# Kernel tuning notes

Measured on AMD Instinct MI355X. Metric: run time of the kernel, lower is better.

## Reference

```python
import jax, jax.numpy as jnp
import numpy as np

N_NODES, N_EDGES, N_GRAPHS = 50000, 800000, 128
D_IN, H1, H2, N_CLASSES = 128, 128, 128, 2
NEG_SLOPE = 0.2  # PyG GATConv default


def setup_inputs() -> dict:
    key = jax.random.key(0)
    ks = jax.random.split(key, 12)
    x = jax.random.normal(ks[0], (N_NODES, D_IN), jnp.float32)
    edge_index = jax.random.randint(ks[1], (2, N_EDGES), 0, N_NODES, jnp.int32)
    batch = jnp.sort(jax.random.randint(ks[2], (N_NODES,), 0, N_GRAPHS, jnp.int32))
    s = 0.05
    return {
        "x": x,
        "W1": jax.random.normal(ks[3], (D_IN, H1), jnp.float32) * s,
        "att_src": jax.random.normal(ks[4], (H1,), jnp.float32) * s,
        "att_dst": jax.random.normal(ks[5], (H1,), jnp.float32) * s,
        "b1": jnp.zeros((H1,), jnp.float32),
        "W2": jax.random.normal(ks[6], (H1, H2), jnp.float32) * s,
        "b2": jnp.zeros((H2,), jnp.float32),
        "Wf": jax.random.normal(ks[7], (H2, N_CLASSES), jnp.float32) * s,
        "bf": jnp.zeros((N_CLASSES,), jnp.float32),
        "edge_index": edge_index,
        "batch": batch,
    }


def _add_self_loops(src, dst, n):
    loop = jnp.arange(n, dtype=src.dtype)
    return jnp.concatenate([src, loop]), jnp.concatenate([dst, loop])


def gat_conv(x, W, att_src, att_dst, bias, src, dst, n):
    h = x @ W  # [N, H1]
    a_src = h @ att_src  # [N]
    a_dst = h @ att_dst  # [N]
    e = a_src[src] + a_dst[dst]  # [E']
    e = jnp.where(e > 0, e, NEG_SLOPE * e)  # leaky_relu
    # softmax over incoming edges of each dst node
    m = jax.ops.segment_max(e, dst, num_segments=n)
    ex = jnp.exp(e - m[dst])
    denom = jax.ops.segment_sum(ex, dst, num_segments=n)
    alpha = ex / denom[dst]  # self loops guarantee denom > 0
    out = jax.ops.segment_sum(alpha[:, None] * h[src], dst, num_segments=n)
    return out + bias


def gcn_conv(x, W, bias, src, dst, n):
    h = x @ W  # [N, H2]
    ones = jnp.ones(src.shape[0], h.dtype)
    deg = jax.ops.segment_sum(ones, dst, num_segments=n)
    dinv = jnp.where(deg > 0, jax.lax.rsqrt(deg), 0.0)
    norm = dinv[src] * dinv[dst]  # [E']
    out = jax.ops.segment_sum(norm[:, None] * h[src], dst, num_segments=n)
    return out + bias


def reference(x, W1, att_src, att_dst, b1, W2, b2, Wf, bf, edge_index, batch):
    n = x.shape[0]
    src, dst = _add_self_loops(edge_index[0], edge_index[1], n)
    h = jax.nn.relu(gat_conv(x, W1, att_src, att_dst, b1, src, dst, n))
    h = jax.nn.relu(gcn_conv(h, W2, b2, src, dst, n))
    # global mean pool over graphs
    sums = jax.ops.segment_sum(h, batch, num_segments=N_GRAPHS)
    cnts = jax.ops.segment_sum(jnp.ones((n,), h.dtype), batch, num_segments=N_GRAPHS)
    rep = sums / jnp.maximum(cnts, 1.0)[:, None]
    return rep @ Wf + bf
```

## Files before the change

### kernel.cpp

```cpp
#include <hip/hip_runtime.h>

#define NN 50000
#define NE 800000
#define EP (NE + NN)
#define NG 128
#define F 128
#define NBE 208
#define EPB 4096
#define NBUCK 196
#define BCAP 6144
#define GB1 782

typedef __attribute__((ext_vector_type(8))) short short8;
typedef __attribute__((ext_vector_type(4))) float float4v;
typedef __attribute__((ext_vector_type(2))) float float2v;
union U8 { uint4 u; short8 s; };

__device__ inline unsigned int bf16rn(float x) {
    unsigned int u = __float_as_uint(x);
    u += 0x7fffu + ((u >> 16) & 1u);
    return u >> 16;
}
__device__ inline unsigned int pack2(float a, float b) {
    return bf16rn(a) | (bf16rn(b) << 16);
}
__device__ inline void bf8_fma2(float2v* acc, float w, uint4 hv) {
    const float2v wv = {w, w};
    float2v p0, p1, p2, p3;
    p0.x = __uint_as_float(hv.x << 16); p0.y = __uint_as_float(hv.x & 0xffff0000u);
    p1.x = __uint_as_float(hv.y << 16); p1.y = __uint_as_float(hv.y & 0xffff0000u);
    p2.x = __uint_as_float(hv.z << 16); p2.y = __uint_as_float(hv.z & 0xffff0000u);
    p3.x = __uint_as_float(hv.w << 16); p3.y = __uint_as_float(hv.w & 0xffff0000u);
    acc[0] += wv * p0;
    acc[1] += wv * p1;
    acc[2] += wv * p2;
    acc[3] += wv * p3;
}

__global__ void pack_wfrag2(const float* __restrict__ W1, const float* __restrict__ W2,
                            uint4* __restrict__ wf, float* __restrict__ gscr,
                            int* __restrict__ cnt) {
    const int p = blockIdx.x * blockDim.x + threadIdx.x;
    if (p >= 4096) {
        const int t = threadIdx.x;
        for (int i = t; i < NG * 32; i += 256) gscr[i] = 0.f;
        for (int i = t; i < NBUCK; i += 256) cnt[i] = 0;
        return;
    }
    const float* W = (p < 2048) ? W1 : W2;
    const int q = p & 2047;
    const int f = q >> 6, l = q & 63;
    const int kt = f >> 3, nt = f & 7;
    const int rb = kt * 32 + ((l >> 4) << 3);
    const int col = nt * 16 + (l & 15);
    const float* wp = W + (size_t)rb * F + col;
    uint4 pk;
    pk.x = pack2(wp[0],     wp[F]);
    pk.y = pack2(wp[2 * F], wp[3 * F]);
    pk.z = pack2(wp[4 * F], wp[5 * F]);
    pk.w = pack2(wp[6 * F], wp[7 * F]);
    wf[p] = pk;
}

__device__ __forceinline__ void gemm1_body(
        const float* __restrict__ Af, const uint4* __restrict__ wf,
        unsigned short* __restrict__ Cb,
        const float* __restrict__ att_src, const float* __restrict__ att_dst,
        float* __restrict__ asrc, float* __restrict__ adst, int bid) {
    const int t = threadIdx.x;
    const int wave = t >> 6, lane = t & 63;
    const int m0 = bid * 64 + wave * 16;
    const int arow = m0 + (lane & 15);
    const int kq = (lane >> 4) << 3;
    U8 a[4];
#pragma unroll
    for (int kt = 0; kt < 4; ++kt) {
        if (arow < NN) {
            const float* ap = Af + (size_t)arow * F + kt * 32 + kq;
            const float4 f0 = *(const float4*)ap;
            const float4 f1 = *(const float4*)(ap + 4);
            a[kt].u = make_uint4(pack2(f0.x, f0.y), pack2(f0.z, f0.w),
                                 pack2(f1.x, f1.y), pack2(f1.z, f1.w));
        } else {
            a[kt].u = make_uint4(0, 0, 0, 0);
        }
    }
    const int ccol = lane & 15;
    const int crow0 = m0 + ((lane >> 4) << 2);
    float ps[4] = {}, pd[4] = {};
    for (int nt = 0; nt < 8; nt += 2) {
        float4v acc0 = {0.f, 0.f, 0.f, 0.f}, acc1 = {0.f, 0.f, 0.f, 0.f};
#pragma unroll
        for (int kt = 0; kt < 4; ++kt) {
            U8 b0, b1;
            b0.u = wf[(kt * 8 + nt) * 64 + lane];
            b1.u = wf[(kt * 8 + nt + 1) * 64 + lane];
            acc0 = __builtin_amdgcn_mfma_f32_16x16x32_bf16(a[kt].s, b0.s, acc0, 0, 0, 0);
            acc1 = __builtin_amdgcn_mfma_f32_16x16x32_bf16(a[kt].s, b1.s, acc1, 0, 0, 0);
        }
#pragma unroll
        for (int r = 0; r < 4; ++r) {
            const int row = crow0 + r;
            if (row < NN) {
                Cb[(size_t)row * F + nt * 16 + ccol]       = (unsigned short)bf16rn(acc0[r]);
                Cb[(size_t)row * F + (nt + 1) * 16 + ccol] = (unsigned short)bf16rn(acc1[r]);
            }
        }
        const float as0 = att_src[nt * 16 + ccol], as1 = att_src[(nt + 1) * 16 + ccol];
        const float ad0 = att_dst[nt * 16 + ccol], ad1 = att_dst[(nt + 1) * 16 + ccol];
#pragma unroll
        for (int r = 0; r < 4; ++r) {
            ps[r] += acc0[r] * as0 + acc1[r] * as1;
            pd[r] += acc0[r] * ad0 + acc1[r] * ad1;
        }
    }
#pragma unroll
    for (int r = 0; r < 4; ++r) {
        float s = ps[r], d = pd[r];
#pragma unroll
        for (int o = 8; o; o >>= 1) { s += __shfl_xor(s, o); d += __shfl_xor(d, o); }
        const int row = crow0 + r;
        if (ccol == 0 && row < NN) { asrc[row] = s; adst[row] = d; }
    }
}

__global__ __launch_bounds__(256) void gemm1_count_scatter(
        const float* __restrict__ x, const uint4* __restrict__ wf1,
        unsigned short* __restrict__ h1b,
        const float* __restrict__ att_src, const float* __restrict__ att_dst,
        float* __restrict__ asrc, float* __restrict__ adst,
        const int* __restrict__ ei, int* __restrict__ cur,
        unsigned int* __restrict__ ebuf) {
    if (blockIdx.x < GB1) {
        gemm1_body(x, wf1, h1b, att_src, att_dst, asrc, adst, blockIdx.x);
        return;
    }
    __shared__ int lcnt[NBUCK];
    __shared__ int lbase[NBUCK];
    const int t = threadIdx.x, b = blockIdx.x - GB1;
    for (int i = t; i < NBUCK; i += 256) lcnt[i] = 0;
    __syncthreads();
    const int e0 = b * EPB;
    int sarr[EPB / 256], darr[EPB / 256];
#pragma unroll
    for (int i = 0; i < EPB / 256; ++i) {
        const int e = e0 + i * 256 + t;
        int s = 0, d = -1;
        if (e < EP) {
            if (e < NE) { s = ei[e]; d = ei[NE + e]; } else { s = d = e - NE; }
            atomicAdd(&lcnt[d >> 8], 1);
        }
        sarr[i] = s; darr[i] = d;
    }
    __syncthreads();
    for (int i = t; i < NBUCK; i += 256) {
        lbase[i] = atomicAdd(&cur[i], lcnt[i]);
        lcnt[i] = 0;
    }
    __syncthreads();
#pragma unroll
    for (int i = 0; i < EPB / 256; ++i) {
        const int d = darr[i];
        if (d >= 0) {
            const int bk = d >> 8;
            const int p = lbase[bk] + atomicAdd(&lcnt[bk], 1);
            ebuf[(size_t)bk * BCAP + p] = (unsigned int)sarr[i] | ((unsigned int)(d & 255) << 16);
        }
    }
}

__global__ __launch_bounds__(256) void bucket_sort(
        const unsigned int* __restrict__ ebuf, const int* __restrict__ cnt,
        const float* __restrict__ asrc, const float* __restrict__ adst,
        int* __restrict__ row_start, uint2* __restrict__ ca,
        unsigned short* __restrict__ csr16,
        int* __restrict__ deg, float* __restrict__ dinv) {
    __shared__ unsigned int earr[BCAP];
    __shared__ float evarr[BCAP];
    __shared__ unsigned short out16[BCAP];
    __shared__ unsigned char dst8[BCAP];
    __shared__ int ecnt[256], epre[256];
    __shared__ float adst_s[256];
    __shared__ float inv_s[256];
    const int t = threadIdx.x, g = blockIdx.x;
    const int m = cnt[g];
    const int n = g * 256 + t;
    adst_s[t] = (n < NN) ? adst[n] : 0.f;
    const unsigned int* src = ebuf + (size_t)g * BCAP;
    ecnt[t] = 0;
    __syncthreads();
    for (int i = t; i < m; i += 256) {
        const unsigned int v = src[i];
        earr[i] = v;
        atomicAdd(&ecnt[v >> 16], 1);
    }
    __syncthreads();
    const int v0 = ecnt[t];
    epre[t] = v0;
    __syncthreads();
    for (int o = 1; o < 256; o <<= 1) {
        const int u = (t >= o) ? epre[t - o] : 0;
        __syncthreads();
        epre[t] += u;
        __syncthreads();
    }
    const int my_excl = epre[t] - v0;
    if (n < NN) {
        row_start[n] = g * BCAP + my_excl;
        deg[n] = v0;
        dinv[n] = rsqrtf((float)v0);
    }
    ecnt[t] = my_excl;
    __syncthreads();
#pragma unroll 4
    for (int i = t; i < m; i += 256) {
        const unsigned int v = earr[i];
        const int s  = (int)(v & 0xffffu);
        const int dl = (int)(v >> 16);
        const int p  = atomicAdd(&ecnt[dl], 1);
        out16[p] = (unsigned short)s;
        dst8[p]  = (unsigned char)dl;
        float sc = asrc[s] + adst_s[dl];
        sc = sc > 0.f ? sc : 0.2f * sc;
        evarr[p] = __expf(sc);
    }
    __syncthreads();
    {
        float den = 0.f;
        for (int k = 0; k < v0; ++k) den += evarr[my_excl + k];
        inv_s[t] = (v0 > 0) ? (1.f / den) : 0.f;
    }
    __syncthreads();
    uint2* cap = ca + (size_t)g * BCAP;
    unsigned short* c16 = csr16 + (size_t)g * BCAP;
    for (int i = t; i < m; i += 256) {
        const unsigned short s = out16[i];
        const float a = evarr[i] * inv_s[dst8[i]];
        cap[i] = make_uint2((unsigned int)s, __float_as_uint(a));
        c16[i] = s;
    }
}

__global__ __launch_bounds__(256) void gat_gemm2(
        const int* __restrict__ row_start, const int* __restrict__ deg,
        const uint2* __restrict__ ca,
        const unsigned short* __restrict__ hb, const float* __restrict__ bias,
        const uint4* __restrict__ wf2, const float* __restrict__ dinv,
        unsigned short* __restrict__ h2b) {
    __shared__ uint4 ldsA[16][17];
    const int lane = threadIdx.x & 63;
    const int qid  = threadIdx.x >> 4;
    const int n    = blockIdx.x * 16 + qid;
    const int lanesub = lane & 15;
    const int qb   = lane & 48;
    const int qo   = lanesub << 3;
    const int lo = row_start[n], hi = lo + deg[n];
    float2v acc[4];
#pragma unroll
    for (int i = 0; i < 4; ++i) acc[i] = (float2v){0.f, 0.f};
    for (int base = lo; base < hi; base += 16) {
        const int cnt = min(16, hi - base);
        int sv = 0; float ev = 0.f;
        if (lanesub < cnt) {
            const uint2 e = ca[base + lanesub];
            sv = (int)e.x; ev = __uint_as_float(e.y);
        }
        for (int j = 0; j < cnt; j += 8) {
            int ss[8]; float ww[8]; uint4 hh[8];
#pragma unroll
            for (int k = 0; k < 8; ++k) {
                ss[k] = __shfl(sv, qb + j + k);
                ww[k] = __shfl(ev, qb + j + k);
            }
#pragma unroll
            for (int k = 0; k < 8; ++k)
                hh[k] = *(const uint4*)(hb + (size_t)ss[k] * F + qo);
#pragma unroll
            for (int k = 0; k < 8; ++k) bf8_fma2(acc, ww[k], hh[k]);
        }
    }
    const float4 b0 = *(const float4*)(bias + qo);
    const float4 b1 = *(const float4*)(bias + qo + 4);
    float v[8];
    v[0] = acc[0].x + b0.x; v[1] = acc[0].y + b0.y;
    v[2] = acc[1].x + b0.z; v[3] = acc[1].y + b0.w;
    v[4] = acc[2].x + b1.x; v[5] = acc[2].y + b1.y;
    v[6] = acc[3].x + b1.z; v[7] = acc[3].y + b1.w;
#pragma unroll
    for (int i = 0; i < 8; ++i) v[i] = v[i] > 0.f ? v[i] : 0.f;
    uint4 pk;
    pk.x = pack2(v[0], v[1]); pk.y = pack2(v[2], v[3]);
    pk.z = pack2(v[4], v[5]); pk.w = pack2(v[6], v[7]);
    ldsA[qid][lanesub] = pk;
    __syncthreads();
    const int wave = threadIdx.x >> 6;
    U8 a[4];
#pragma unroll
    for (int kt = 0; kt < 4; ++kt)
        a[kt].u = ldsA[lane & 15][kt * 4 + (lane >> 4)];
    const int nt = wave * 2;
    float4v acc0 = {0.f, 0.f, 0.f, 0.f}, acc1 = {0.f, 0.f, 0.f, 0.f};
#pragma unroll
    for (int kt = 0; kt < 4; ++kt) {
        U8 b0f, b1f;
        b0f.u = wf2[(kt * 8 + nt) * 64 + lane];
        b1f.u = wf2[(kt * 8 + nt + 1) * 64 + lane];
        acc0 = __builtin_amdgcn_mfma_f32_16x16x32_bf16(a[kt].s, b0f.s, acc0, 0, 0, 0);
        acc1 = __builtin_amdgcn_mfma_f32_16x16x32_bf16(a[kt].s, b1f.s, acc1, 0, 0, 0);
    }
    const int ccol = lane & 15;
    const int crow0 = (lane >> 4) << 2;
#pragma unroll
    for (int r = 0; r < 4; ++r) {
        const int node = blockIdx.x * 16 + crow0 + r;
        const float rs = dinv[node];
        h2b[(size_t)node * F + nt * 16 + ccol]       = (unsigned short)bf16rn(acc0[r] * rs);
        h2b[(size_t)node * F + (nt + 1) * 16 + ccol] = (unsigned short)bf16rn(acc1[r] * rs);
    }
}

__global__ __launch_bounds__(256) void gcn_gather_pool(
        const int* __restrict__ row_start, const int* __restrict__ deg,
        const unsigned short* __restrict__ csr_src,
        const float* __restrict__ dinv, const unsigned short* __restrict__ hb,
        const float* __restrict__ bias, const int* __restrict__ batch,
        const float* __restrict__ Wf, float* __restrict__ gscr) {
    __shared__ int   sg[16];
    __shared__ float sp0[16], sp1[16];
    const int lane = threadIdx.x & 63;
    const int qid  = threadIdx.x >> 4;
    const int n    = blockIdx.x * 16 + qid;
    const int lanesub = lane & 15;
    const int qb   = lane & 48;
    const int qo   = lanesub << 3;
    const int lo = row_start[n], hi = lo + deg[n];
    const float dn = dinv[n];
    float2v acc[4];
#pragma unroll
    for (int i = 0; i < 4; ++i) acc[i] = (float2v){0.f, 0.f};
    for (int base = lo; base < hi; base += 16) {
        const int cnt = min(16, hi - base);
        int sv = 0;
        if (lanesub < cnt) sv = (int)csr_src[base + lanesub];
        for (int j = 0; j < cnt; j += 8) {
            int ss[8]; uint4 hh[8];
#pragma unroll
            for (int k = 0; k < 8; ++k) ss[k] = __shfl(sv, qb + j + k);
#pragma unroll
            for (int k = 0; k < 8; ++k)
                hh[k] = *(const uint4*)(hb + (size_t)ss[k] * F + qo);
#pragma unroll
            for (int k = 0; k < 8; ++k) {
                const float w = (j + k < cnt) ? 1.f : 0.f;
                bf8_fma2(acc, w, hh[k]);
            }
        }
    }
    const float4 b0 = *(const float4*)(bias + qo);
    const float4 b1 = *(const float4*)(bias + qo + 4);
    float v[8];
    v[0] = fmaf(acc[0].x, dn, b0.x); v[1] = fmaf(acc[0].y, dn, b0.y);
    v[2] = fmaf(acc[1].x, dn, b0.z); v[3] = fmaf(acc[1].y, dn, b0.w);
    v[4] = fmaf(acc[2].x, dn, b1.x); v[5] = fmaf(acc[2].y, dn, b1.y);
    v[6] = fmaf(acc[3].x, dn, b1.z); v[7] = fmaf(acc[3].y, dn, b1.w);
#pragma unroll
    for (int i = 0; i < 8; ++i) v[i] = v[i] > 0.f ? v[i] : 0.f;
    const float4 w0 = *(const float4*)(Wf + qo * 2);
    const float4 w1 = *(const float4*)(Wf + qo * 2 + 4);
    const float4 w2 = *(const float4*)(Wf + qo * 2 + 8);
    const float4 w3 = *(const float4*)(Wf + qo * 2 + 12);
    float p0 = v[0]*w0.x + v[1]*w0.z + v[2]*w1.x + v[3]*w1.z +
               v[4]*w2.x + v[5]*w2.z + v[6]*w3.x + v[7]*w3.z;
    float p1 = v[0]*w0.y + v[1]*w0.w + v[2]*w1.y + v[3]*w1.w +
               v[4]*w2.y + v[5]*w2.w + v[6]*w3.y + v[7]*w3.w;
#pragma unroll
    for (int o = 8; o; o >>= 1) { p0 += __shfl_xor(p0, o); p1 += __shfl_xor(p1, o); }
    if (lanesub == 0) { sg[qid] = batch[n]; sp0[qid] = p0; sp1[qid] = p1; }
    __syncthreads();
    if (threadIdx.x == 0) {
#pragma unroll 1
        for (int w = 0; w < 16; ++w) {
            const int g = sg[w];
            if (g < 0) continue;
            float q0 = sp0[w], q1 = sp1[w];
            for (int u = w + 1; u < 16; ++u) {
                if (sg[u] == g) { q0 += sp0[u]; q1 += sp1[u]; sg[u] = -1; }
            }
            atomicAdd(gscr + g * 32,     q0);
            atomicAdd(gscr + g * 32 + 1, q1);
        }
    }
}

__global__ void finalize(const float* __restrict__ gscr, const int* __restrict__ batch,
                         const float* __restrict__ bf, float* __restrict__ out) {
    const int g = threadIdx.x;
    int lo = 0, hi = NN;
    while (lo < hi) { int m = (lo + hi) >> 1; if (batch[m] < g) lo = m + 1; else hi = m; }
    int lo2 = lo, hi2 = NN;
    while (lo2 < hi2) { int m = (lo2 + hi2) >> 1; if (batch[m] < g + 1) lo2 = m + 1; else hi2 = m; }
    const float inv = 1.f / fmaxf((float)(lo2 - lo), 1.f);
    out[g * 2]     = gscr[g * 32]     * inv + bf[0];
    out[g * 2 + 1] = gscr[g * 32 + 1] * inv + bf[1];
}

extern "C" void kernel_launch(void* const* d_in, const int* in_sizes, int n_in,
                              void* d_out, int out_size, void* d_ws, size_t ws_size,
                              hipStream_t stream) {
    const float* x       = (const float*)d_in[0];
    const float* W1      = (const float*)d_in[1];
    const float* att_src = (const float*)d_in[2];
    const float* att_dst = (const float*)d_in[3];
    const float* b1      = (const float*)d_in[4];
    const float* W2      = (const float*)d_in[5];
    const float* b2      = (const float*)d_in[6];
    const float* Wf      = (const float*)d_in[7];
    const float* bf      = (const float*)d_in[8];
    const int*   ei      = (const int*)d_in[9];
    const int*   batch   = (const int*)d_in[10];
    float* out = (float*)d_out;

    uint4* wf1       = (uint4*)d_ws;
    uint4* wf2       = wf1 + 2048;
    uint2* ca        = (uint2*)(wf2 + 2048);
    unsigned int* ebuf = (unsigned int*)(ca + (size_t)NBUCK * BCAP);
    unsigned short* h1b = (unsigned short*)(ebuf + (size_t)NBUCK * BCAP);
    unsigned short* h2b = h1b + (size_t)NN * F;
    unsigned short* csr16 = h2b + (size_t)NN * F;
    float* asrc      = (float*)(csr16 + (size_t)NBUCK * BCAP);
    float* adst      = asrc + NN;
    float* dinv      = adst + NN;
    float* gscr      = dinv + NN;
    int*   row_start = (int*)(gscr + NG * 32);
    int*   deg       = row_start + NN;
    int*   cnt       = deg + NN;

    pack_wfrag2<<<17, 256, 0, stream>>>(W1, W2, wf1, gscr, cnt);
    gemm1_count_scatter<<<GB1 + NBE, 256, 0, stream>>>(x, wf1, h1b, att_src, att_dst,
                                                       asrc, adst, ei, cnt, ebuf);
    bucket_sort<<<NBUCK, 256, 0, stream>>>(ebuf, cnt, asrc, adst,
                                           row_start, ca, csr16, deg, dinv);
    gat_gemm2<<<NN / 16, 256, 0, stream>>>(row_start, deg, ca, h1b, b1, wf2, dinv, h2b);
    gcn_gather_pool<<<NN / 16, 256, 0, stream>>>(row_start, deg, csr16, dinv, h2b, b2,
                                                 batch, Wf, gscr);
    finalize<<<1, NG, 0, stream>>>(gscr, batch, bf, out);
}
```

Measured before the change: 190.5 us.

## Store intermediate node features h1/h2 in FP8 with interleaved channel layout

The bf16 hidden-feature buffers produced by the first GEMM and the second GEMM are replaced with FP8 (e4m3) storage. Channels are permuted so each lane's 8 consecutive bytes hold channels j*16+lane, and W2 fragments are repacked to match that layout. The gather loops in gat_gemm2 and gcn_gather_pool now issue 8-byte loads, fetch both 8-edge groups before accumulating, and decode with hardware cvt_pk_f32_fp8. This halves the bytes moved by the bandwidth-bound random neighbour gathers, at the cost of reduced precision that may exceed the tolerance.

```diff
diff --git a/kernel.cpp b/kernel.cpp
--- a/kernel.cpp
+++ b/kernel.cpp
@@ -24,13 +24,12 @@
 __device__ inline unsigned int pack2(float a, float b) {
     return bf16rn(a) | (bf16rn(b) << 16);
 }
-__device__ inline void bf8_fma2(float2v* acc, float w, uint4 hv) {
+__device__ inline void fp8_fma2(float2v* acc, float w, uint2 hv) {
     const float2v wv = {w, w};
-    float2v p0, p1, p2, p3;
-    p0.x = __uint_as_float(hv.x << 16); p0.y = __uint_as_float(hv.x & 0xffff0000u);
-    p1.x = __uint_as_float(hv.y << 16); p1.y = __uint_as_float(hv.y & 0xffff0000u);
-    p2.x = __uint_as_float(hv.z << 16); p2.y = __uint_as_float(hv.z & 0xffff0000u);
-    p3.x = __uint_as_float(hv.w << 16); p3.y = __uint_as_float(hv.w & 0xffff0000u);
+    float2v p0 = __builtin_amdgcn_cvt_pk_f32_fp8((int)hv.x, false);
+    float2v p1 = __builtin_amdgcn_cvt_pk_f32_fp8((int)hv.x, true);
+    float2v p2 = __builtin_amdgcn_cvt_pk_f32_fp8((int)hv.y, false);
+    float2v p3 = __builtin_amdgcn_cvt_pk_f32_fp8((int)hv.y, true);
     acc[0] += wv * p0;
     acc[1] += wv * p1;
     acc[2] += wv * p2;
@@ -47,24 +46,32 @@
         for (int i = t; i < NBUCK; i += 256) cnt[i] = 0;
         return;
     }
-    const float* W = (p < 2048) ? W1 : W2;
     const int q = p & 2047;
     const int f = q >> 6, l = q & 63;
     const int kt = f >> 3, nt = f & 7;
     const int rb = kt * 32 + ((l >> 4) << 3);
     const int col = nt * 16 + (l & 15);
-    const float* wp = W + (size_t)rb * F + col;
     uint4 pk;
-    pk.x = pack2(wp[0],     wp[F]);
-    pk.y = pack2(wp[2 * F], wp[3 * F]);
-    pk.z = pack2(wp[4 * F], wp[5 * F]);
-    pk.w = pack2(wp[6 * F], wp[7 * F]);
+    if (p < 2048) {
+        const float* wp = W1 + (size_t)rb * F + col;
+        pk.x = pack2(wp[0],     wp[F]);
+        pk.y = pack2(wp[2 * F], wp[3 * F]);
+        pk.z = pack2(wp[4 * F], wp[5 * F]);
+        pk.w = pack2(wp[6 * F], wp[7 * F]);
+    } else {
+        const int rbs = rb >> 3;
+        const float* wp = W2 + (size_t)rbs * F + col;
+        pk.x = pack2(wp[(size_t)0 * 16 * F], wp[(size_t)1 * 16 * F]);
+        pk.y = pack2(wp[(size_t)2 * 16 * F], wp[(size_t)3 * 16 * F]);
+        pk.z = pack2(wp[(size_t)4 * 16 * F], wp[(size_t)5 * 16 * F]);
+        pk.w = pack2(wp[(size_t)6 * 16 * F], wp[(size_t)7 * 16 * F]);
+    }
     wf[p] = pk;
 }
 
 __device__ __forceinline__ void gemm1_body(
         const float* __restrict__ Af, const uint4* __restrict__ wf,
-        unsigned short* __restrict__ Cb,
+        uint2* __restrict__ Cb8,
         const float* __restrict__ att_src, const float* __restrict__ att_dst,
         float* __restrict__ asrc, float* __restrict__ adst, int bid) {
     const int t = threadIdx.x;
@@ -88,7 +95,10 @@
     const int ccol = lane & 15;
     const int crow0 = m0 + ((lane >> 4) << 2);
     float ps[4] = {}, pd[4] = {};
-    for (int nt = 0; nt < 8; nt += 2) {
+    int plo[4] = {0, 0, 0, 0}, phi[4] = {0, 0, 0, 0};
+#pragma unroll
+    for (int ntp = 0; ntp < 4; ++ntp) {
+        const int nt = ntp * 2;
         float4v acc0 = {0.f, 0.f, 0.f, 0.f}, acc1 = {0.f, 0.f, 0.f, 0.f};
 #pragma unroll
         for (int kt = 0; kt < 4; ++kt) {
@@ -100,11 +110,10 @@
         }
 #pragma unroll
         for (int r = 0; r < 4; ++r) {
-            const int row = crow0 + r;
-            if (row < NN) {
-                Cb[(size_t)row * F + nt * 16 + ccol]       = (unsigned short)bf16rn(acc0[r]);
-                Cb[(size_t)row * F + (nt + 1) * 16 + ccol] = (unsigned short)bf16rn(acc1[r]);
-            }
+            if (ntp == 0)      plo[r] = __builtin_amdgcn_cvt_pk_fp8_f32(acc0[r], acc1[r], plo[r], false);
+            else if (ntp == 1) plo[r] = __builtin_amdgcn_cvt_pk_fp8_f32(acc0[r], acc1[r], plo[r], true);
+            else if (ntp == 2) phi[r] = __builtin_amdgcn_cvt_pk_fp8_f32(acc0[r], acc1[r], phi[r], false);
+            else               phi[r] = __builtin_amdgcn_cvt_pk_fp8_f32(acc0[r], acc1[r], phi[r], true);
         }
         const float as0 = att_src[nt * 16 + ccol], as1 = att_src[(nt + 1) * 16 + ccol];
         const float ad0 = att_dst[nt * 16 + ccol], ad1 = att_dst[(nt + 1) * 16 + ccol];
@@ -116,6 +125,12 @@
     }
 #pragma unroll
     for (int r = 0; r < 4; ++r) {
+        const int row = crow0 + r;
+        if (row < NN)
+            Cb8[(size_t)row * 16 + ccol] = make_uint2((unsigned)plo[r], (unsigned)phi[r]);
+    }
+#pragma unroll
+    for (int r = 0; r < 4; ++r) {
         float s = ps[r], d = pd[r];
 #pragma unroll
         for (int o = 8; o; o >>= 1) { s += __shfl_xor(s, o); d += __shfl_xor(d, o); }
@@ -126,7 +141,7 @@
 
 __global__ __launch_bounds__(256) void gemm1_count_scatter(
         const float* __restrict__ x, const uint4* __restrict__ wf1,
-        unsigned short* __restrict__ h1b,
+        uint2* __restrict__ h1b,
         const float* __restrict__ att_src, const float* __restrict__ att_dst,
         float* __restrict__ asrc, float* __restrict__ adst,
         const int* __restrict__ ei, int* __restrict__ cur,
@@ -244,16 +259,16 @@
 __global__ __launch_bounds__(256) void gat_gemm2(
         const int* __restrict__ row_start, const int* __restrict__ deg,
         const uint2* __restrict__ ca,
-        const unsigned short* __restrict__ hb, const float* __restrict__ bias,
+        const unsigned char* __restrict__ hb, const float* __restrict__ bias,
         const uint4* __restrict__ wf2, const float* __restrict__ dinv,
-        unsigned short* __restrict__ h2b) {
+        unsigned char* __restrict__ h2b) {
     __shared__ uint4 ldsA[16][17];
     const int lane = threadIdx.x & 63;
     const int qid  = threadIdx.x >> 4;
     const int n    = blockIdx.x * 16 + qid;
     const int lanesub = lane & 15;
     const int qb   = lane & 48;
-    const int qo   = lanesub << 3;
+    const int qo8  = lanesub << 3;
     const int lo = row_start[n], hi = lo + deg[n];
     float2v acc[4];
 #pragma unroll
@@ -265,29 +280,43 @@
             const uint2 e = ca[base + lanesub];
             sv = (int)e.x; ev = __uint_as_float(e.y);
         }
-        for (int j = 0; j < cnt; j += 8) {
-            int ss[8]; float ww[8]; uint4 hh[8];
+        int ss0[8]; float ww0[8]; uint2 hh0[8], hh1[8];
+#pragma unroll
+        for (int k = 0; k < 8; ++k) {
+            ss0[k] = __shfl(sv, qb + k);
+            ww0[k] = __shfl(ev, qb + k);
+        }
+#pragma unroll
+        for (int k = 0; k < 8; ++k)
+            hh0[k] = *(const uint2*)(hb + (size_t)ss0[k] * F + qo8);
+        const bool g1 = cnt > 8;
+        float ww1[8];
+        if (g1) {
+            int ss1[8];
 #pragma unroll
             for (int k = 0; k < 8; ++k) {
-                ss[k] = __shfl(sv, qb + j + k);
-                ww[k] = __shfl(ev, qb + j + k);
+                ss1[k] = __shfl(sv, qb + 8 + k);
+                ww1[k] = __shfl(ev, qb + 8 + k);
             }
 #pragma unroll
             for (int k = 0; k < 8; ++k)
-                hh[k] = *(const uint4*)(hb + (size_t)ss[k] * F + qo);
-#pragma unroll
-            for (int k = 0; k < 8; ++k) bf8_fma2(acc, ww[k], hh[k]);
-        }
-    }
-    const float4 b0 = *(const float4*)(bias + qo);
-    const float4 b1 = *(const float4*)(bias + qo + 4);
+                hh1[k] = *(const uint2*)(hb + (size_t)ss1[k] * F + qo8);
+        }
+#pragma unroll
+        for (int k = 0; k < 8; ++k) fp8_fma2(acc, ww0[k], hh0[k]);
+        if (g1) {
+#pragma unroll
+            for (int k = 0; k < 8; ++k) fp8_fma2(acc, ww1[k], hh1[k]);
+        }
+    }
     float v[8];
-    v[0] = acc[0].x + b0.x; v[1] = acc[0].y + b0.y;
-    v[2] = acc[1].x + b0.z; v[3] = acc[1].y + b0.w;
-    v[4] = acc[2].x + b1.x; v[5] = acc[2].y + b1.y;
-    v[6] = acc[3].x + b1.z; v[7] = acc[3].y + b1.w;
-#pragma unroll
-    for (int i = 0; i < 8; ++i) v[i] = v[i] > 0.f ? v[i] : 0.f;
+#pragma unroll
+    for (int j = 0; j < 4; ++j) { v[2 * j] = acc[j].x; v[2 * j + 1] = acc[j].y; }
+#pragma unroll
+    for (int j = 0; j < 8; ++j) {
+        const float tv = v[j] + bias[j * 16 + lanesub];
+        v[j] = tv > 0.f ? tv : 0.f;
+    }
     uint4 pk;
     pk.x = pack2(v[0], v[1]); pk.y = pack2(v[2], v[3]);
     pk.z = pack2(v[4], v[5]); pk.w = pack2(v[6], v[7]);
@@ -314,15 +343,15 @@
     for (int r = 0; r < 4; ++r) {
         const int node = blockIdx.x * 16 + crow0 + r;
         const float rs = dinv[node];
-        h2b[(size_t)node * F + nt * 16 + ccol]       = (unsigned short)bf16rn(acc0[r] * rs);
-        h2b[(size_t)node * F + (nt + 1) * 16 + ccol] = (unsigned short)bf16rn(acc1[r] * rs);
+        const int pk8 = __builtin_amdgcn_cvt_pk_fp8_f32(acc0[r] * rs, acc1[r] * rs, 0, false);
+        *(unsigned short*)(h2b + (size_t)node * F + ccol * 8 + nt) = (unsigned short)pk8;
     }
 }
 
 __global__ __launch_bounds__(256) void gcn_gather_pool(
         const int* __restrict__ row_start, const int* __restrict__ deg,
         const unsigned short* __restrict__ csr_src,
-        const float* __restrict__ dinv, const unsigned short* __restrict__ hb,
+        const float* __restrict__ dinv, const unsigned char* __restrict__ hb,
         const float* __restrict__ bias, const int* __restrict__ batch,
         const float* __restrict__ Wf, float* __restrict__ gscr) {
     __shared__ int   sg[16];
@@ -332,7 +361,7 @@
     const int n    = blockIdx.x * 16 + qid;
     const int lanesub = lane & 15;
     const int qb   = lane & 48;
-    const int qo   = lanesub << 3;
+    const int qo8  = lanesub << 3;
     const int lo = row_start[n], hi = lo + deg[n];
     const float dn = dinv[n];
     float2v acc[4];
@@ -342,37 +371,43 @@
         const int cnt = min(16, hi - base);
         int sv = 0;
         if (lanesub < cnt) sv = (int)csr_src[base + lanesub];
-        for (int j = 0; j < cnt; j += 8) {
-            int ss[8]; uint4 hh[8];
-#pragma unroll
-            for (int k = 0; k < 8; ++k) ss[k] = __shfl(sv, qb + j + k);
+        int ss0[8]; uint2 hh0[8], hh1[8];
+#pragma unroll
+        for (int k = 0; k < 8; ++k) ss0[k] = __shfl(sv, qb + k);
+#pragma unroll
+        for (int k = 0; k < 8; ++k)
+            hh0[k] = *(const uint2*)(hb + (size_t)ss0[k] * F + qo8);
+        const bool g1 = cnt > 8;
+        if (g1) {
+            int ss1[8];
+#pragma unroll
+            for (int k = 0; k < 8; ++k) ss1[k] = __shfl(sv, qb + 8 + k);
 #pragma unroll
             for (int k = 0; k < 8; ++k)
-                hh[k] = *(const uint4*)(hb + (size_t)ss[k] * F + qo);
-#pragma unroll
-            for (int k = 0; k < 8; ++k) {
-                const float w = (j + k < cnt) ? 1.f : 0.f;
-                bf8_fma2(acc, w, hh[k]);
-            }
-        }
-    }
-    const float4 b0 = *(const float4*)(bias + qo);
-    const float4 b1 = *(const float4*)(bias + qo + 4);
+                hh1[k] = *(const uint2*)(hb + (size_t)ss1[k] * F + qo8);
+        }
+#pragma unroll
+        for (int k = 0; k < 8; ++k)
+            fp8_fma2(acc, (k < cnt) ? 1.f : 0.f, hh0[k]);
+        if (g1) {
+#pragma unroll
+            for (int k = 0; k < 8; ++k)
+                fp8_fma2(acc, (8 + k < cnt) ? 1.f : 0.f, hh1[k]);
+        }
+    }
     float v[8];
-    v[0] = fmaf(acc[0].x, dn, b0.x); v[1] = fmaf(acc[0].y, dn, b0.y);
-    v[2] = fmaf(acc[1].x, dn, b0.z); v[3] = fmaf(acc[1].y, dn, b0.w);
-    v[4] = fmaf(acc[2].x, dn, b1.x); v[5] = fmaf(acc[2].y, dn, b1.y);
-    v[6] = fmaf(acc[3].x, dn, b1.z); v[7] = fmaf(acc[3].y, dn, b1.w);
-#pragma unroll
-    for (int i = 0; i < 8; ++i) v[i] = v[i] > 0.f ? v[i] : 0.f;
-    const float4 w0 = *(const float4*)(Wf + qo * 2);
-    const float4 w1 = *(const float4*)(Wf + qo * 2 + 4);
-    const float4 w2 = *(const float4*)(Wf + qo * 2 + 8);
-    const float4 w3 = *(const float4*)(Wf + qo * 2 + 12);
-    float p0 = v[0]*w0.x + v[1]*w0.z + v[2]*w1.x + v[3]*w1.z +
-               v[4]*w2.x + v[5]*w2.z + v[6]*w3.x + v[7]*w3.z;
-    float p1 = v[0]*w0.y + v[1]*w0.w + v[2]*w1.y + v[3]*w1.w +
-               v[4]*w2.y + v[5]*w2.w + v[6]*w3.y + v[7]*w3.w;
+#pragma unroll
+    for (int j = 0; j < 4; ++j) { v[2 * j] = acc[j].x; v[2 * j + 1] = acc[j].y; }
+    float p0 = 0.f, p1 = 0.f;
+#pragma unroll
+    for (int j = 0; j < 8; ++j) {
+        const int ch = j * 16 + lanesub;
+        float tv = fmaf(v[j], dn, bias[ch]);
+        tv = tv > 0.f ? tv : 0.f;
+        const float2 wv = *(const float2*)(Wf + (ch << 1));
+        p0 += tv * wv.x;
+        p1 += tv * wv.y;
+    }
 #pragma unroll
     for (int o = 8; o; o >>= 1) { p0 += __shfl_xor(p0, o); p1 += __shfl_xor(p1, o); }
     if (lanesub == 0) { sg[qid] = batch[n]; sp0[qid] = p0; sp1[qid] = p1; }
@@ -424,9 +459,9 @@
     uint4* wf2       = wf1 + 2048;
     uint2* ca        = (uint2*)(wf2 + 2048);
     unsigned int* ebuf = (unsigned int*)(ca + (size_t)NBUCK * BCAP);
-    unsigned short* h1b = (unsigned short*)(ebuf + (size_t)NBUCK * BCAP);
-    unsigned short* h2b = h1b + (size_t)NN * F;
-    unsigned short* csr16 = h2b + (size_t)NN * F;
+    unsigned char* h1b = (unsigned char*)(ebuf + (size_t)NBUCK * BCAP);
+    unsigned char* h2b = h1b + (size_t)NN * F;
+    unsigned short* csr16 = (unsigned short*)(h2b + (size_t)NN * F);
     float* asrc      = (float*)(csr16 + (size_t)NBUCK * BCAP);
     float* adst      = asrc + NN;
     float* dinv      = adst + NN;
@@ -436,7 +471,7 @@
     int*   cnt       = deg + NN;
 
     pack_wfrag2<<<17, 256, 0, stream>>>(W1, W2, wf1, gscr, cnt);
-    gemm1_count_scatter<<<GB1 + NBE, 256, 0, stream>>>(x, wf1, h1b, att_src, att_dst,
+    gemm1_count_scatter<<<GB1 + NBE, 256, 0, stream>>>(x, wf1, (uint2*)h1b, att_src, att_dst,
                                                        asrc, adst, ei, cnt, ebuf);
     bucket_sort<<<NBUCK, 256, 0, stream>>>(ebuf, cnt, asrc, adst,
                                            row_start, ca, csr16, deg, dinv);
```

Result: faster. 171.6 us (-9.9%).
